# Optimization experiments

Hardware: AMD Instinct MI355X
Metric: run time of the kernel (lower is better)

## Reference

```python
import jax, jax.numpy as jnp
import numpy as np
from jax import lax

# Constants (canonical show-attend-tell values)
ENCODER_DIM = 2048
ATTENTION_DIM = 512
DECODER_DIM = 512
EMBED_DIM = 512
VOCAB = 10000
B, L, T = 64, 196, 32


def setup_inputs() -> dict:
    key = jax.random.key(0)
    ks = jax.random.split(key, 20)
    s = 0.02
    inp = {
        "encoder_out": jax.random.normal(ks[0], (B, L, ENCODER_DIM), jnp.float32),
        "captions": jax.random.randint(ks[1], (B, T), 0, VOCAB),
        "lengths": jax.random.randint(ks[2], (B,), 2, T + 1).at[0].set(T),
        # parameters (stored as [in, out] for x @ W)
        "emb_table": jax.random.normal(ks[3], (VOCAB, EMBED_DIM), jnp.float32) * s,
        "W_a": jax.random.normal(ks[4], (ENCODER_DIM, ATTENTION_DIM), jnp.float32) * s,
        "U_a": jax.random.normal(ks[5], (DECODER_DIM, ATTENTION_DIM), jnp.float32) * s,
        "w_att": jax.random.normal(ks[6], (ATTENTION_DIM,), jnp.float32) * s,
        "fb_W": jax.random.normal(ks[7], (DECODER_DIM, 1), jnp.float32) * s,
        "fb_b": jnp.zeros((1,), jnp.float32),
        "W_ih": jax.random.normal(ks[8], (4 * DECODER_DIM, EMBED_DIM + ENCODER_DIM), jnp.float32) * s,
        "W_hh": jax.random.normal(ks[9], (4 * DECODER_DIM, DECODER_DIM), jnp.float32) * s,
        "b_ih": jnp.zeros((4 * DECODER_DIM,), jnp.float32),
        "b_hh": jnp.zeros((4 * DECODER_DIM,), jnp.float32),
        "fc_W": jax.random.normal(ks[10], (DECODER_DIM, VOCAB), jnp.float32) * s,
        "fc_b": jnp.zeros((VOCAB,), jnp.float32),
        "ih_W": jax.random.normal(ks[11], (ENCODER_DIM, DECODER_DIM), jnp.float32) * s,
        "ih_b": jnp.zeros((DECODER_DIM,), jnp.float32),
        "ic_W": jax.random.normal(ks[12], (ENCODER_DIM, DECODER_DIM), jnp.float32) * s,
        "ic_b": jnp.zeros((DECODER_DIM,), jnp.float32),
    }
    return inp


def reference(encoder_out, captions, lengths, emb_table, W_a, U_a, w_att,
              fb_W, fb_b, W_ih, W_hh, b_ih, b_hh, fc_W, fc_b,
              ih_W, ih_b, ic_W, ic_b):
    # sort by descending length (as in original)
    sort_idx = jnp.argsort(-lengths)
    enc = encoder_out[sort_idx]          # [B, L, D_enc]
    caps = captions[sort_idx]            # [B, T]
    dl = lengths[sort_idx] - 1           # decode lengths, max == T-1 by construction
    max_t = caps.shape[1] - 1

    emb = emb_table[caps]                # [B, T, E]
    mean = enc.mean(axis=1)
    h0 = jnp.tanh(mean @ ih_W + ih_b)    # [B, H]
    c0 = jnp.tanh(mean @ ic_W + ic_b)

    Wa_enc = enc @ W_a                   # [B, L, A], precomputed once

    def step(carry, xs):
        h, c = carry
        e_t, mask = xs                   # [B, E], [B] bool (dl > t)
        att = jnp.tanh(Wa_enc + (h @ U_a)[:, None, :])        # [B, L, A]
        energy = jnp.einsum('bla,a->bl', att, w_att)          # [B, L]
        alpha = jax.nn.softmax(energy, axis=1)
        context = jnp.einsum('bl,ble->be', alpha, enc)        # [B, D_enc]
        beta = jax.nn.sigmoid(h @ fb_W + fb_b)                # [B, 1]
        context = beta * context
        x = jnp.concatenate([e_t, context], axis=1)           # [B, E+D_enc]
        gates = x @ W_ih.T + b_ih + h @ W_hh.T + b_hh         # [B, 4H]
        i, f, g, o = jnp.split(gates, 4, axis=1)
        i = jax.nn.sigmoid(i); f = jax.nn.sigmoid(f)
        g = jnp.tanh(g); o = jax.nn.sigmoid(o)
        c_new = f * c + i * g
        h_new = o * jnp.tanh(c_new)
        m = mask[:, None]
        h2 = jnp.where(m, h_new, h)
        c2 = jnp.where(m, c_new, c)
        pred = jnp.where(m, h_new @ fc_W + fc_b, 0.0)         # [B, V]
        a_out = jnp.where(m, alpha, 0.0)
        return (h2, c2), (pred, a_out)

    xs = (emb[:, :max_t].transpose(1, 0, 2),                  # [T-1, B, E]
          jnp.arange(max_t)[:, None] < dl[None, :])           # [T-1, B]
    _, (preds, alphas) = lax.scan(step, (h0, c0), xs)
    predictions = preds.transpose(1, 0, 2)                    # [B, T-1, V]
    alphas = alphas.transpose(1, 0, 2)                        # [B, T-1, L]
    return predictions, caps, dl, alphas, sort_idx
```

## Files before the change

kernel.cpp:

```cpp
#include <hip/hip_runtime.h>
#include <cstdint>
#include <cstddef>

#define BB 64
#define LL 196
#define EE 2048
#define AD 512
#define DD 512
#define EM 512
#define VV 10000
#define TTOK 32
#define MT 31
#define KX 3072
#define G4 2048
#define VPAD 10048

#define OUT_PRED 0
#define OUT_CAPS (BB*MT*VV)
#define OUT_DL   (OUT_CAPS + BB*TTOK)
#define OUT_ALPH (OUT_DL + BB)
#define OUT_SIDX (OUT_ALPH + BB*MT*LL)

#define OFF_SIDX 0
#define OFF_DL   64
#define OFF_MEAN 128
#define OFF_C    (OFF_MEAN + BB*EE)
#define OFF_HU   (OFF_C + BB*DD)
#define OFF_ATT  (OFF_HU + BB*AD)
#define OFF_GACC (OFF_ATT + BB*256)
#define OFF_HB   (OFF_GACC + BB*G4)
#define OFF_XFB  (OFF_HB + BB*DD/2)
#define OFF_WB   (OFF_XFB + BB*KX/2)
#define OFF_FCWB (OFF_WB + (size_t)G4*KX/2)
#define OFF_UAB  (OFF_FCWB + (size_t)VPAD*DD/2)
#define OFF_WAB  (OFF_UAB + (size_t)AD*DD/2)
#define OFF_WAEB (OFF_WAB + (size_t)AD*EE/2)
#define OFF_EBF  (OFF_WAEB + (size_t)BB*LL*AD/2)
#define OFF_MEANB OFF_WAEB
#define OFF_IHB  (OFF_WAEB + 65536)
#define OFF_ICB  (OFF_WAEB + 65536 + 524288)

typedef unsigned short u16;
typedef __attribute__((ext_vector_type(8))) short bf16x8;
typedef __attribute__((ext_vector_type(4))) float f32x4;
#define MFMA16(a,b,c) __builtin_amdgcn_mfma_f32_16x16x32_bf16(a,b,c,0,0,0)

__device__ inline u16 f2bf(float x){
    unsigned u = __float_as_uint(x);
    unsigned r = (u + 0x7FFFu + ((u >> 16) & 1u)) >> 16;
    return (u16)r;
}
__device__ inline float bf2f(u16 x){ return __uint_as_float(((unsigned)x) << 16); }
__device__ inline float sigm(float x){ return 1.0f/(1.0f + __expf(-x)); }
__device__ inline float ftanh(float x){ return 2.0f/(1.0f + __expf(-2.0f*x)) - 1.0f; }

__device__ inline void gload16(const u16* g, u16* l){
    __builtin_amdgcn_global_load_lds((const __attribute__((address_space(1))) void*)g,
                                     (__attribute__((address_space(3))) void*)l, 16, 0, 0);
}

__global__ void k_sort(const int* __restrict__ lengths, const int* __restrict__ captions,
                       float* __restrict__ out, int* __restrict__ sidx, int* __restrict__ dl){
    __shared__ int len_s[BB];
    __shared__ int pos_s[BB];
    int i = threadIdx.x;
    len_s[i] = lengths[i];
    __syncthreads();
    int li = len_s[i];
    int rank = 0;
    for (int j = 0; j < BB; j++){
        int lj = len_s[j];
        rank += (lj > li) || (lj == li && j < i);
    }
    pos_s[rank] = i;
    __syncthreads();
    int src = pos_s[i];
    sidx[i] = src;
    int d = len_s[src] - 1;
    dl[i] = d;
    out[OUT_SIDX + i] = (float)src;
    out[OUT_DL + i]   = (float)d;
    for (int t = 0; t < TTOK; t++)
        out[OUT_CAPS + i*TTOK + t] = (float)captions[src*TTOK + t];
}

__global__ void k_ginit(float* __restrict__ gacc, float* __restrict__ mean){
    int gid = blockIdx.x*256 + threadIdx.x;
    if (gid < 65536) gacc[gid] = 0.f;
    else mean[gid - 65536] = 0.f;
}

__global__ void k_meanbf(const float* __restrict__ enc, const int* __restrict__ sidx,
                         float* __restrict__ mean, u16* __restrict__ ebf){
    int b = blockIdx.y;
    int e = (blockIdx.x*256 + threadIdx.x)*4;
    int l0 = blockIdx.z*98, l1 = l0 + 98;
    int src = sidx[b];
    const float* p = enc + (size_t)src*LL*EE + e;
    u16* o = ebf + (size_t)b*LL*EE + e;
    float sx = 0.f, sy = 0.f, sz = 0.f, sw = 0.f;
    for (int l = l0; l < l1; l++){
        float4 v = *(const float4*)(p + (size_t)l*EE);
        sx += v.x; sy += v.y; sz += v.z; sw += v.w;
        unsigned lo = (unsigned)f2bf(v.x) | ((unsigned)f2bf(v.y) << 16);
        unsigned hi = (unsigned)f2bf(v.z) | ((unsigned)f2bf(v.w) << 16);
        uint2 pk; pk.x = lo; pk.y = hi;
        *(uint2*)(o + (size_t)l*EE) = pk;
    }
    atomicAdd(&mean[b*EE + e + 0], sx);
    atomicAdd(&mean[b*EE + e + 1], sy);
    atomicAdd(&mean[b*EE + e + 2], sz);
    atomicAdd(&mean[b*EE + e + 3], sw);
}

__global__ void k_meanb(const float* __restrict__ mean, u16* __restrict__ meanb){
    int i = (blockIdx.x*256 + threadIdx.x)*8;
    float4 a = *(const float4*)(mean + i);
    float4 b = *(const float4*)(mean + i + 4);
    const float s = 1.0f/196.0f;
    uint4 pk;
    pk.x = (unsigned)f2bf(a.x*s) | ((unsigned)f2bf(a.y*s) << 16);
    pk.y = (unsigned)f2bf(a.z*s) | ((unsigned)f2bf(a.w*s) << 16);
    pk.z = (unsigned)f2bf(b.x*s) | ((unsigned)f2bf(b.y*s) << 16);
    pk.w = (unsigned)f2bf(b.z*s) | ((unsigned)f2bf(b.w*s) << 16);
    *(uint4*)(meanb + i) = pk;
}

__global__ void k_wb(const float* __restrict__ W_ih, const float* __restrict__ W_hh,
                     u16* __restrict__ Wb){
    int n = blockIdx.y;
    int k = blockIdx.x*256 + threadIdx.x;
    float v = (k < 2560) ? W_ih[(size_t)n*2560 + k] : W_hh[(size_t)n*512 + (k - 2560)];
    Wb[(size_t)n*KX + k] = f2bf(v);
}

__global__ void k_tr(const float* __restrict__ in, u16* __restrict__ out, int K, int N){
    __shared__ float tile[32][33];
    int k0 = blockIdx.x*32, n0 = blockIdx.y*32;
    int tx = threadIdx.x, ty = threadIdx.y;
    for (int r = ty; r < 32; r += 8){
        int k = k0 + r, n = n0 + tx;
        tile[r][tx] = (n < N) ? in[(size_t)k*N + n] : 0.f;
    }
    __syncthreads();
    for (int r = ty; r < 32; r += 8){
        int n = n0 + r, k = k0 + tx;
        out[(size_t)n*K + k] = f2bf(tile[tx][r]);
    }
}

__global__ void k_h0c0s(const u16* __restrict__ ihb, const u16* __restrict__ icb,
                        const u16* __restrict__ meanb, float* __restrict__ hc){
    int tid = threadIdx.x, lane = tid & 63, w = tid >> 6;
    int lane15 = lane & 15, quad = lane >> 4;
    int z = blockIdx.y;
    int ks = blockIdx.z;
    const u16* Wm = z ? icb : ihb;
    int n0 = blockIdx.x*64 + w*16;
    const u16* bp = Wm + (size_t)(n0 + lane15)*EE + ks*512 + quad*8;
    const u16* ap = meanb + (size_t)lane15*EE + ks*512 + quad*8;
    f32x4 zz = {0.f,0.f,0.f,0.f};
    f32x4 acc[4] = {zz,zz,zz,zz};
    #pragma unroll 4
    for (int kc = 0; kc < 16; kc++){
        bf16x8 bv = *(const bf16x8*)(bp + kc*32);
        bf16x8 a0 = *(const bf16x8*)(ap + kc*32);
        bf16x8 a1 = *(const bf16x8*)(ap + 16*EE + kc*32);
        bf16x8 a2 = *(const bf16x8*)(ap + 32*EE + kc*32);
        bf16x8 a3 = *(const bf16x8*)(ap + 48*EE + kc*32);
        acc[0] = MFMA16(a0, bv, acc[0]);
        acc[1] = MFMA16(a1, bv, acc[1]);
        acc[2] = MFMA16(a2, bv, acc[2]);
        acc[3] = MFMA16(a3, bv, acc[3]);
    }
    int j = n0 + lane15;
    #pragma unroll
    for (int mt = 0; mt < 4; mt++)
        #pragma unroll
        for (int r = 0; r < 4; r++){
            int m = mt*16 + quad*4 + r;
            atomicAdd(&hc[z*32768 + m*512 + j], acc[mt][r]);
        }
}

__global__ void k_h0c0f(float* __restrict__ gacc, const float* __restrict__ ih_b,
                        const float* __restrict__ ic_b, const float* __restrict__ b_ih,
                        const float* __restrict__ b_hh, u16* __restrict__ hb,
                        float* __restrict__ c, u16* __restrict__ xfb){
    int gid = blockIdx.x*256 + threadIdx.x;
    if (gid < 65536){
        int z = gid >> 15;
        int mj = gid & 32767;
        int m = mj >> 9, j = mj & 511;
        float v = tanhf(gacc[gid] + (z ? ic_b[j] : ih_b[j]));
        if (z == 0){
            u16 hv = f2bf(v);
            hb[m*DD + j] = hv;
            xfb[(size_t)m*KX + 2560 + j] = hv;
        } else {
            c[m*DD + j] = v;
        }
    }
    int jj = gid & (G4-1);
    gacc[gid] = b_ih[jj] + b_hh[jj];
}

#define BKK 64
__global__ __launch_bounds__(256) void k_waenc2(const u16* __restrict__ ebf,
                                                const u16* __restrict__ Wab,
                                                u16* __restrict__ Waeb){
    __shared__ __align__(16) u16 As[2][128*BKK];
    __shared__ __align__(16) u16 Bs[2][128*BKK];
    int tid = threadIdx.x, lane = tid & 63, w = tid >> 6;
    int lane15 = lane & 15, quad = lane >> 4;
    int m0 = blockIdx.x * 128;
    int n0 = blockIdx.y * 128;

    int srow = w*8 + (lane >> 3);
    int scol = 8 * ((lane & 7) ^ (lane >> 3));
    const u16* ag = ebf + (size_t)(m0 + srow)*EE + scol;
    const u16* bg = Wab + (size_t)(n0 + srow)*EE + scol;

    f32x4 zz = {0.f,0.f,0.f,0.f};
    f32x4 acc[4][4];
    #pragma unroll
    for (int mt = 0; mt < 4; mt++)
        #pragma unroll
        for (int nt = 0; nt < 4; nt++) acc[mt][nt] = zz;

    int ar  = (w >> 1) * 64;
    int brr = (w & 1) * 64;
    int rx  = (lane15 & 7) << 3;

    {
        u16* la = &As[0][w*512 + lane*8];
        u16* lb = &Bs[0][w*512 + lane*8];
        #pragma unroll
        for (int i = 0; i < 4; i++){
            gload16(ag + (size_t)(i*32)*EE, la + i*2048);
            gload16(bg + (size_t)(i*32)*EE, lb + i*2048);
        }
    }
    __syncthreads();

    int cur = 0;
    for (int kt = 0; kt < 32; kt++){
        if (kt < 31){
            u16* la = &As[cur^1][w*512 + lane*8];
            u16* lb = &Bs[cur^1][w*512 + lane*8];
            const u16* a = ag + (size_t)(kt+1)*BKK;
            const u16* b = bg + (size_t)(kt+1)*BKK;
            #pragma unroll
            for (int i = 0; i < 4; i++){
                gload16(a + (size_t)(i*32)*EE, la + i*2048);
                gload16(b + (size_t)(i*32)*EE, lb + i*2048);
            }
        }
        bf16x8 af[4][2], bfr[4][2];
        #pragma unroll
        for (int mt = 0; mt < 4; mt++)
            #pragma unroll
            for (int ks = 0; ks < 2; ks++){
                af[mt][ks]  = *(const bf16x8*)&As[cur][(ar  + mt*16 + lane15)*BKK + ((ks*32 + quad*8) ^ rx)];
                bfr[mt][ks] = *(const bf16x8*)&Bs[cur][(brr + mt*16 + lane15)*BKK + ((ks*32 + quad*8) ^ rx)];
            }
        #pragma unroll
        for (int ks = 0; ks < 2; ks++)
            #pragma unroll
            for (int mt = 0; mt < 4; mt++)
                #pragma unroll
                for (int nt = 0; nt < 4; nt++)
                    acc[mt][nt] = MFMA16(af[mt][ks], bfr[nt][ks], acc[mt][nt]);
        __syncthreads();
        cur ^= 1;
    }

    #pragma unroll
    for (int mt = 0; mt < 4; mt++)
        #pragma unroll
        for (int nt = 0; nt < 4; nt++)
            #pragma unroll
            for (int r = 0; r < 4; r++){
                int row = m0 + ar + mt*16 + quad*4 + r;
                Waeb[(size_t)row*AD + n0 + brr + nt*16 + lane15] = f2bf(acc[mt][nt][r]);
            }
}

__global__ __launch_bounds__(256) void k_energyA(const u16* __restrict__ Waeb,
                       const float* __restrict__ hU, const float* __restrict__ w_att,
                       float* __restrict__ en){
    int tid = threadIdx.x, lane = tid & 63, w = tid >> 6;
    int b = blockIdx.x >> 2, sub = blockIdx.x & 3;

    const float* hub = hU + (size_t)b*AD;
    float hw[8], ww[8];
    #pragma unroll
    for (int ii = 0; ii < 8; ii++){
        hw[ii] = hub[ii*64 + lane];
        ww[ii] = w_att[ii*64 + lane];
    }
    int l0 = sub*49;
    for (int l = l0 + w; l < l0 + 49; l += 4){
        const u16* wa = Waeb + ((size_t)b*LL + l)*AD;
        float acc = 0.f;
        #pragma unroll
        for (int ii = 0; ii < 8; ii++)
            acc += ftanh(bf2f(wa[ii*64 + lane]) + hw[ii]) * ww[ii];
        #pragma unroll
        for (int off = 32; off; off >>= 1) acc += __shfl_xor(acc, off, 64);
        if (lane == 0) en[b*256 + l] = acc;
    }
}

__global__ __launch_bounds__(256) void k_ctx(const float* __restrict__ en,
                      const u16* __restrict__ ebf, const u16* __restrict__ hb,
                      const float* __restrict__ fb_W, const float* __restrict__ fb_b,
                      const float* __restrict__ emb_table, const int* __restrict__ captions,
                      const int* __restrict__ sidx, const int* __restrict__ dl,
                      u16* __restrict__ xfb, float* __restrict__ out, int t){
    __shared__ float red[256];
    __shared__ float alpha_s[LL];
    __shared__ float sbeta;
    int b = blockIdx.y, q = blockIdx.x, tid = threadIdx.x;

    float e = (tid < LL) ? en[b*256 + tid] : -3.0e38f;
    red[tid] = e; __syncthreads();
    for (int s = 128; s > 0; s >>= 1){ if (tid < s) red[tid] = fmaxf(red[tid], red[tid+s]); __syncthreads(); }
    float mx = red[0]; __syncthreads();
    float p = (tid < LL) ? __expf(e - mx) : 0.f;
    red[tid] = p; __syncthreads();
    for (int s = 128; s > 0; s >>= 1){ if (tid < s) red[tid] += red[tid+s]; __syncthreads(); }
    float ssum = red[0]; __syncthreads();
    float alpha = p / ssum;
    if (tid < LL){
        alpha_s[tid] = alpha;
        if (q == 0)
            out[OUT_ALPH + ((size_t)b*MT + t)*LL + tid] = (t < dl[b]) ? alpha : 0.f;
    }

    red[tid] = bf2f(hb[b*DD + tid]) * fb_W[tid]
             + bf2f(hb[b*DD + 256 + tid]) * fb_W[256 + tid];
    __syncthreads();
    for (int s = 128; s > 0; s >>= 1){ if (tid < s) red[tid] += red[tid+s]; __syncthreads(); }
    if (tid == 0) sbeta = sigm(red[0] + fb_b[0]);

    int cap = captions[sidx[b]*TTOK + t];
    if (tid < 128)
        xfb[(size_t)b*KX + q*128 + tid] = f2bf(emb_table[(size_t)cap*EM + q*128 + tid]);
    __syncthreads();

    float beta = sbeta;
    int e0 = q*512 + tid*2;
    const u16* pe = ebf + (size_t)b*LL*EE + e0;
    float ax = 0.f, ay = 0.f;
    for (int l = 0; l < LL; l++){
        unsigned u = *(const unsigned*)(pe + (size_t)l*EE);
        float a = alpha_s[l];
        ax += a * __uint_as_float(u << 16);
        ay += a * __uint_as_float(u & 0xFFFF0000u);
    }
    unsigned pk = (unsigned)f2bf(beta*ax) | ((unsigned)f2bf(beta*ay) << 16);
    *(unsigned*)(xfb + (size_t)b*KX + EM + e0) = pk;
}

__global__ void k_gates(const u16* __restrict__ Wb, const u16* __restrict__ xfb,
                        float* __restrict__ gacc){
    int tid = threadIdx.x, lane = tid & 63, w = tid >> 6;
    int lane15 = lane & 15, quad = lane >> 4;
    int n0 = blockIdx.x*64 + w*16;
    int kbase = blockIdx.y*384;
    const u16* bp = Wb + (size_t)(n0 + lane15)*KX + kbase + quad*8;
    const u16* ap = xfb + (size_t)lane15*KX + kbase + quad*8;
    f32x4 z = {0.f,0.f,0.f,0.f};
    f32x4 acc[4] = {z,z,z,z};
    #pragma unroll 4
    for (int kc = 0; kc < 12; kc++){
        bf16x8 bv = *(const bf16x8*)(bp + kc*32);
        bf16x8 a0 = *(const bf16x8*)(ap + kc*32);
        bf16x8 a1 = *(const bf16x8*)(ap + 16*KX + kc*32);
        bf16x8 a2 = *(const bf16x8*)(ap + 32*KX + kc*32);
        bf16x8 a3 = *(const bf16x8*)(ap + 48*KX + kc*32);
        acc[0] = MFMA16(a0, bv, acc[0]);
        acc[1] = MFMA16(a1, bv, acc[1]);
        acc[2] = MFMA16(a2, bv, acc[2]);
        acc[3] = MFMA16(a3, bv, acc[3]);
    }
    #pragma unroll
    for (int mt = 0; mt < 4; mt++)
        #pragma unroll
        for (int r = 0; r < 4; r++){
            int m = mt*16 + quad*4 + r;
            atomicAdd(&gacc[(size_t)m*G4 + n0 + lane15], acc[mt][r]);
        }
}

__global__ void k_update(float* __restrict__ gacc, const float* __restrict__ b_ih,
                         const float* __restrict__ b_hh, const int* __restrict__ dl,
                         u16* __restrict__ hb, float* __restrict__ c,
                         u16* __restrict__ xfb, int t){
    int gid = blockIdx.x*256 + threadIdx.x;
    int b = gid >> 9, d = gid & 511;
    size_t base = (size_t)b*G4 + d;
    float gi = gacc[base];
    float gf = gacc[base + 512];
    float gg = gacc[base + 1024];
    float go = gacc[base + 1536];
    float ig = sigm(gi), fg = sigm(gf), g = ftanh(gg), o = sigm(go);
    float cold = c[gid];
    float cn = fg*cold + ig*g;
    float hn = o*ftanh(cn);
    if (t < dl[b]){
        c[gid] = cn;
        u16 hv = f2bf(hn);
        hb[gid] = hv;
        xfb[(size_t)b*KX + 2560 + d] = hv;
    }
    gacc[base]        = b_ih[d]        + b_hh[d];
    gacc[base + 512]  = b_ih[d + 512]  + b_hh[d + 512];
    gacc[base + 1024] = b_ih[d + 1024] + b_hh[d + 1024];
    gacc[base + 1536] = b_ih[d + 1536] + b_hh[d + 1536];
}

__global__ void k_pred(const u16* __restrict__ fcWb, const float* __restrict__ fc_b,
                       const u16* __restrict__ Uab, const u16* __restrict__ hb,
                       const int* __restrict__ dl, float* __restrict__ out,
                       float* __restrict__ hU, int t, int hu_only){
    int tid = threadIdx.x, lane = tid & 63, w = tid >> 6;
    int lane15 = lane & 15, quad = lane >> 4;
    int bid = blockIdx.x;
    bool pred; int jc;
    if (hu_only){ pred = false; jc = bid; }
    else if (bid < 157){ pred = true; jc = bid; }
    else { pred = false; jc = bid - 157; }
    const u16* W = pred ? fcWb : Uab;
    int n0 = jc*64 + w*16;
    const u16* bp = W + (size_t)(n0 + lane15)*AD + quad*8;
    const u16* ap = hb + (size_t)lane15*AD + quad*8;
    f32x4 z = {0.f,0.f,0.f,0.f};
    f32x4 acc[4] = {z,z,z,z};
    #pragma unroll 4
    for (int kc = 0; kc < 16; kc++){
        bf16x8 bv = *(const bf16x8*)(bp + kc*32);
        bf16x8 a0 = *(const bf16x8*)(ap + kc*32);
        bf16x8 a1 = *(const bf16x8*)(ap + 16*AD + kc*32);
        bf16x8 a2 = *(const bf16x8*)(ap + 32*AD + kc*32);
        bf16x8 a3 = *(const bf16x8*)(ap + 48*AD + kc*32);
        acc[0] = MFMA16(a0, bv, acc[0]);
        acc[1] = MFMA16(a1, bv, acc[1]);
        acc[2] = MFMA16(a2, bv, acc[2]);
        acc[3] = MFMA16(a3, bv, acc[3]);
    }
    if (pred){
        int j = n0 + lane15;
        if (j < VV){
            float bias = fc_b[j];
            #pragma unroll
            for (int mt = 0; mt < 4; mt++)
                #pragma unroll
                for (int r = 0; r < 4; r++){
                    int b = mt*16 + quad*4 + r;
                    bool mk = t < dl[b];
                    out[OUT_PRED + ((size_t)b*MT + t)*VV + j] = mk ? acc[mt][r] + bias : 0.f;
                }
        }
    } else {
        int n = n0 + lane15;
        #pragma unroll
        for (int mt = 0; mt < 4; mt++)
            #pragma unroll
            for (int r = 0; r < 4; r++){
                int b = mt*16 + quad*4 + r;
                hU[(size_t)b*AD + n] = acc[mt][r];
            }
    }
}

extern "C" void kernel_launch(void* const* d_in, const int* in_sizes, int n_in,
                              void* d_out, int out_size, void* d_ws, size_t ws_size,
                              hipStream_t stream) {
    const float* enc       = (const float*)d_in[0];
    const int*   captions  = (const int*)d_in[1];
    const int*   lengths   = (const int*)d_in[2];
    const float* emb_table = (const float*)d_in[3];
    const float* W_a       = (const float*)d_in[4];
    const float* U_a       = (const float*)d_in[5];
    const float* w_att     = (const float*)d_in[6];
    const float* fb_W      = (const float*)d_in[7];
    const float* fb_b      = (const float*)d_in[8];
    const float* W_ih      = (const float*)d_in[9];
    const float* W_hh      = (const float*)d_in[10];
    const float* b_ih      = (const float*)d_in[11];
    const float* b_hh      = (const float*)d_in[12];
    const float* fc_W      = (const float*)d_in[13];
    const float* fc_b      = (const float*)d_in[14];
    const float* ih_W      = (const float*)d_in[15];
    const float* ih_b      = (const float*)d_in[16];
    const float* ic_W      = (const float*)d_in[17];
    const float* ic_b      = (const float*)d_in[18];

    float* out = (float*)d_out;
    float* ws  = (float*)d_ws;
    int* sidx = (int*)(ws + OFF_SIDX);
    int* dl   = (int*)(ws + OFF_DL);
    float* mean = ws + OFF_MEAN;
    float* c    = ws + OFF_C;
    float* hU   = ws + OFF_HU;
    float* en   = ws + OFF_ATT;
    float* gacc = ws + OFF_GACC;
    u16* hb   = (u16*)(ws + OFF_HB);
    u16* xfb  = (u16*)(ws + OFF_XFB);
    u16* Wb   = (u16*)(ws + OFF_WB);
    u16* fcWb = (u16*)(ws + OFF_FCWB);
    u16* Uab  = (u16*)(ws + OFF_UAB);
    u16* Wab  = (u16*)(ws + OFF_WAB);
    u16* Waeb = (u16*)(ws + OFF_WAEB);
    u16* ebf  = (u16*)(ws + OFF_EBF);
    u16* meanb = (u16*)(ws + OFF_MEANB);
    u16* ihb  = (u16*)(ws + OFF_IHB);
    u16* icb  = (u16*)(ws + OFF_ICB);

    k_sort<<<1, 64, 0, stream>>>(lengths, captions, out, sidx, dl);
    k_ginit<<<768, 256, 0, stream>>>(gacc, mean);
    k_meanbf<<<dim3(2, BB, 2), 256, 0, stream>>>(enc, sidx, mean, ebf);
    k_meanb<<<64, 256, 0, stream>>>(mean, meanb);
    k_tr<<<dim3(64, 16), dim3(32, 8), 0, stream>>>(ih_W, ihb, 2048, 512);
    k_tr<<<dim3(64, 16), dim3(32, 8), 0, stream>>>(ic_W, icb, 2048, 512);
    k_h0c0s<<<dim3(8, 2, 4), 256, 0, stream>>>(ihb, icb, meanb, gacc);
    k_h0c0f<<<512, 256, 0, stream>>>(gacc, ih_b, ic_b, b_ih, b_hh, hb, c, xfb);
    k_wb<<<dim3(12, G4), 256, 0, stream>>>(W_ih, W_hh, Wb);
    k_tr<<<dim3(16, 314), dim3(32, 8), 0, stream>>>(fc_W, fcWb, 512, VV);
    k_tr<<<dim3(16, 16),  dim3(32, 8), 0, stream>>>(U_a, Uab, 512, 512);
    k_tr<<<dim3(64, 16),  dim3(32, 8), 0, stream>>>(W_a, Wab, 2048, 512);
    k_waenc2<<<dim3(98, 4), 256, 0, stream>>>(ebf, Wab, Waeb);
    k_pred<<<8, 256, 0, stream>>>(fcWb, fc_b, Uab, hb, dl, out, hU, 0, 1);

    for (int t = 0; t < MT; t++){
        k_energyA<<<256, 256, 0, stream>>>(Waeb, hU, w_att, en);
        k_ctx<<<dim3(4, BB), 256, 0, stream>>>(en, ebf, hb, fb_W, fb_b,
                                               emb_table, captions, sidx, dl, xfb, out, t);
        k_gates<<<dim3(32, 8), 256, 0, stream>>>(Wb, xfb, gacc);
        k_update<<<128, 256, 0, stream>>>(gacc, b_ih, b_hh, dl, hb, c, xfb, t);
        k_pred<<<165, 256, 0, stream>>>(fcWb, fc_b, Uab, hb, dl, out, hU, t, 0);
    }
}
```

Before: 2.229 ms.

## Batch vocab projection across eight steps and fuse hU into LSTM update

Hidden states from each step are staged in a ring buffer of up to eight slots, which reuses the workspace that held the encoder mean. The fc vocab projection then runs as one batched launch covering up to eight timesteps, pulling this large GEMM out of the serial per-step chain and giving it a much wider grid. The attention projection h·U_a is computed inside the LSTM update kernel with a per-thread scalar dot product over shared-memory h, removing one launch per step. In exchange, that hU dot product runs on only 64 blocks without MFMA, and its per-thread row reads of U_a are strided.

```diff
diff --git a/kernel.cpp b/kernel.cpp
--- a/kernel.cpp
+++ b/kernel.cpp
@@ -394,13 +394,17 @@
         }
 }
 
-__global__ void k_update(float* __restrict__ gacc, const float* __restrict__ b_ih,
-                         const float* __restrict__ b_hh, const int* __restrict__ dl,
-                         u16* __restrict__ hb, float* __restrict__ c,
-                         u16* __restrict__ xfb, int t){
-    int gid = blockIdx.x*256 + threadIdx.x;
-    int b = gid >> 9, d = gid & 511;
+__global__ __launch_bounds__(512) void k_updhu(float* __restrict__ gacc,
+                         const float* __restrict__ b_ih, const float* __restrict__ b_hh,
+                         const int* __restrict__ dl, u16* __restrict__ hb,
+                         float* __restrict__ c, u16* __restrict__ xfb,
+                         const u16* __restrict__ Uab, u16* __restrict__ hall,
+                         float* __restrict__ hU, int t){
+    __shared__ float hs[DD];
+    int b = blockIdx.x, tid = threadIdx.x;
+    int d = tid;
     size_t base = (size_t)b*G4 + d;
+    int gid = b*DD + d;
     float gi = gacc[base];
     float gf = gacc[base + 512];
     float gg = gacc[base + 1024];
@@ -409,9 +413,13 @@
     float cold = c[gid];
     float cn = fg*cold + ig*g;
     float hn = o*ftanh(cn);
-    if (t < dl[b]){
+    bool mk = t < dl[b];
+    float h2 = mk ? hn : bf2f(hb[gid]);
+    hs[d] = h2;
+    u16 hv = f2bf(h2);
+    hall[((size_t)(t & 7)*BB + b)*DD + d] = hv;
+    if (mk){
         c[gid] = cn;
-        u16 hv = f2bf(hn);
         hb[gid] = hv;
         xfb[(size_t)b*KX + 2560 + d] = hv;
     }
@@ -419,22 +427,65 @@
     gacc[base + 512]  = b_ih[d + 512]  + b_hh[d + 512];
     gacc[base + 1024] = b_ih[d + 1024] + b_hh[d + 1024];
     gacc[base + 1536] = b_ih[d + 1536] + b_hh[d + 1536];
-}
-
-__global__ void k_pred(const u16* __restrict__ fcWb, const float* __restrict__ fc_b,
-                       const u16* __restrict__ Uab, const u16* __restrict__ hb,
-                       const int* __restrict__ dl, float* __restrict__ out,
-                       float* __restrict__ hU, int t, int hu_only){
+    __syncthreads();
+    if (t == MT-1) return;
+
+    const u16* up = Uab + (size_t)tid*AD;
+    float acc = 0.f;
+    #pragma unroll 8
+    for (int dd = 0; dd < DD; dd += 8){
+        bf16x8 uv = *(const bf16x8*)(up + dd);
+        #pragma unroll
+        for (int j2 = 0; j2 < 8; j2++)
+            acc += bf2f((u16)uv[j2]) * hs[dd + j2];
+    }
+    hU[(size_t)b*AD + tid] = acc;
+}
+
+__global__ void k_predg(const u16* __restrict__ fcWb, const float* __restrict__ fc_b,
+                        const u16* __restrict__ hall, const int* __restrict__ dl,
+                        float* __restrict__ out, int tbase){
     int tid = threadIdx.x, lane = tid & 63, w = tid >> 6;
     int lane15 = lane & 15, quad = lane >> 4;
-    int bid = blockIdx.x;
-    bool pred; int jc;
-    if (hu_only){ pred = false; jc = bid; }
-    else if (bid < 157){ pred = true; jc = bid; }
-    else { pred = false; jc = bid - 157; }
-    const u16* W = pred ? fcWb : Uab;
+    int jc = blockIdx.x, tloc = blockIdx.y;
+    int tt = tbase + tloc;
     int n0 = jc*64 + w*16;
-    const u16* bp = W + (size_t)(n0 + lane15)*AD + quad*8;
+    const u16* bp = fcWb + (size_t)(n0 + lane15)*AD + quad*8;
+    const u16* ap = hall + (size_t)tloc*BB*DD + (size_t)lane15*AD + quad*8;
+    f32x4 z = {0.f,0.f,0.f,0.f};
+    f32x4 acc[4] = {z,z,z,z};
+    #pragma unroll 4
+    for (int kc = 0; kc < 16; kc++){
+        bf16x8 bv = *(const bf16x8*)(bp + kc*32);
+        bf16x8 a0 = *(const bf16x8*)(ap + kc*32);
+        bf16x8 a1 = *(const bf16x8*)(ap + 16*AD + kc*32);
+        bf16x8 a2 = *(const bf16x8*)(ap + 32*AD + kc*32);
+        bf16x8 a3 = *(const bf16x8*)(ap + 48*AD + kc*32);
+        acc[0] = MFMA16(a0, bv, acc[0]);
+        acc[1] = MFMA16(a1, bv, acc[1]);
+        acc[2] = MFMA16(a2, bv, acc[2]);
+        acc[3] = MFMA16(a3, bv, acc[3]);
+    }
+    int j = n0 + lane15;
+    if (j < VV){
+        float bias = fc_b[j];
+        #pragma unroll
+        for (int mt = 0; mt < 4; mt++)
+            #pragma unroll
+            for (int r = 0; r < 4; r++){
+                int b = mt*16 + quad*4 + r;
+                bool mk = tt < dl[b];
+                out[OUT_PRED + ((size_t)b*MT + tt)*VV + j] = mk ? acc[mt][r] + bias : 0.f;
+            }
+    }
+}
+
+__global__ void k_hu0(const u16* __restrict__ Uab, const u16* __restrict__ hb,
+                      float* __restrict__ hU){
+    int tid = threadIdx.x, lane = tid & 63, w = tid >> 6;
+    int lane15 = lane & 15, quad = lane >> 4;
+    int n0 = blockIdx.x*64 + w*16;
+    const u16* bp = Uab + (size_t)(n0 + lane15)*AD + quad*8;
     const u16* ap = hb + (size_t)lane15*AD + quad*8;
     f32x4 z = {0.f,0.f,0.f,0.f};
     f32x4 acc[4] = {z,z,z,z};
@@ -450,29 +501,14 @@
         acc[2] = MFMA16(a2, bv, acc[2]);
         acc[3] = MFMA16(a3, bv, acc[3]);
     }
-    if (pred){
-        int j = n0 + lane15;
-        if (j < VV){
-            float bias = fc_b[j];
-            #pragma unroll
-            for (int mt = 0; mt < 4; mt++)
-                #pragma unroll
-                for (int r = 0; r < 4; r++){
-                    int b = mt*16 + quad*4 + r;
-                    bool mk = t < dl[b];
-                    out[OUT_PRED + ((size_t)b*MT + t)*VV + j] = mk ? acc[mt][r] + bias : 0.f;
-                }
-        }
-    } else {
-        int n = n0 + lane15;
-        #pragma unroll
-        for (int mt = 0; mt < 4; mt++)
-            #pragma unroll
-            for (int r = 0; r < 4; r++){
-                int b = mt*16 + quad*4 + r;
-                hU[(size_t)b*AD + n] = acc[mt][r];
-            }
-    }
+    int n = n0 + lane15;
+    #pragma unroll
+    for (int mt = 0; mt < 4; mt++)
+        #pragma unroll
+        for (int r = 0; r < 4; r++){
+            int b = mt*16 + quad*4 + r;
+            hU[(size_t)b*AD + n] = acc[mt][r];
+        }
 }
 
 extern "C" void kernel_launch(void* const* d_in, const int* in_sizes, int n_in,
@@ -503,6 +539,7 @@
     int* sidx = (int*)(ws + OFF_SIDX);
     int* dl   = (int*)(ws + OFF_DL);
     float* mean = ws + OFF_MEAN;
+    u16* hall = (u16*)(ws + OFF_MEAN);
     float* c    = ws + OFF_C;
     float* hU   = ws + OFF_HU;
     float* en   = ws + OFF_ATT;
@@ -532,14 +569,17 @@
     k_tr<<<dim3(16, 16),  dim3(32, 8), 0, stream>>>(U_a, Uab, 512, 512);
     k_tr<<<dim3(64, 16),  dim3(32, 8), 0, stream>>>(W_a, Wab, 2048, 512);
     k_waenc2<<<dim3(98, 4), 256, 0, stream>>>(ebf, Wab, Waeb);
-    k_pred<<<8, 256, 0, stream>>>(fcWb, fc_b, Uab, hb, dl, out, hU, 0, 1);
+    k_hu0<<<8, 256, 0, stream>>>(Uab, hb, hU);
 
     for (int t = 0; t < MT; t++){
         k_energyA<<<256, 256, 0, stream>>>(Waeb, hU, w_att, en);
         k_ctx<<<dim3(4, BB), 256, 0, stream>>>(en, ebf, hb, fb_W, fb_b,
                                                emb_table, captions, sidx, dl, xfb, out, t);
         k_gates<<<dim3(32, 8), 256, 0, stream>>>(Wb, xfb, gacc);
-        k_update<<<128, 256, 0, stream>>>(gacc, b_ih, b_hh, dl, hb, c, xfb, t);
-        k_pred<<<165, 256, 0, stream>>>(fcWb, fc_b, Uab, hb, dl, out, hU, t, 0);
-    }
-}
+        k_updhu<<<64, 512, 0, stream>>>(gacc, b_ih, b_hh, dl, hb, c, xfb, Uab, hall, hU, t);
+        if ((t & 7) == 7 || t == MT-1){
+            int tbase = t & ~7;
+            k_predg<<<dim3(157, t - tbase + 1), 256, 0, stream>>>(fcWb, fc_b, hall, dl, out, tbase);
+        }
+    }
+}
```

New measurement: 2.348 ms. +5.4%, slower.
